# Kernel optimization log

Hardware: AMD Instinct MI355X
Metric: run time of the kernel (lower is better)

## Reference

```python
import jax, jax.numpy as jnp
from jax import lax
import numpy as np

INPUT_SIZE, HIDDEN_SIZE, OUTPUT_SIZE = 256, 2048, 128
NUM_STEPS = 8192
ALPHA = 0.1


def setup_inputs() -> dict:
    key = jax.random.key(0)
    ks = jax.random.split(key, 8)
    s_i = 1.0 / np.sqrt(INPUT_SIZE)
    s_h = 1.0 / np.sqrt(HIDDEN_SIZE)
    return {
        "input_sig": jax.random.normal(ks[0], (INPUT_SIZE, NUM_STEPS), jnp.float32),
        "rate": jax.random.uniform(ks[1], (HIDDEN_SIZE,), jnp.float32, -1.0, 1.0),
        "Wi": jax.random.uniform(ks[2], (HIDDEN_SIZE, INPUT_SIZE), jnp.float32, -s_i, s_i),
        "bi": jax.random.uniform(ks[3], (HIDDEN_SIZE,), jnp.float32, -s_i, s_i),
        "Wh": jax.random.uniform(ks[4], (HIDDEN_SIZE, HIDDEN_SIZE), jnp.float32, -s_h, s_h),
        "bh": jax.random.uniform(ks[5], (HIDDEN_SIZE,), jnp.float32, -s_h, s_h),
        "Wo": jax.random.uniform(ks[6], (OUTPUT_SIZE, HIDDEN_SIZE), jnp.float32, -s_h, s_h),
        "bo": jax.random.uniform(ks[7], (OUTPUT_SIZE,), jnp.float32, -s_h, s_h),
    }


def reference(input_sig, rate, Wi, bi, Wh, bh, Wo, bo):
    # Precompute input projection for all steps at once: (T, H)
    xproj = input_sig.T @ Wi.T + bi  # einsum 'ti,hi->th'

    def step(r, xp):
        r_new = jnp.tanh(xp + r @ Wh.T + bh)
        r = (1.0 - ALPHA) * r + ALPHA * r_new
        return r, r

    _, rates = lax.scan(step, rate, xproj)  # rates: (T, H)
    rate_all = rates.T                      # (H, T), matches torch stack(dim=1)
    logits = rates @ Wo.T + bo              # (T, O)
    output = jax.nn.log_softmax(logits.T, axis=0)  # LogSoftmax over classes
    return output, rate_all
```

## Files before the change

kernel.cpp:

```cpp
#include <hip/hip_runtime.h>
#include <math.h>

#define T_STEPS 8192
#define HID     2048
#define IN_SZ   256
#define OUT_SZ  128
#define NBLK    64
#define NTHR    512
#define RPB     32
#define SCRUB   0xFFFFFFFF00000000ull

typedef unsigned long long u64;
typedef unsigned int u32;
typedef __attribute__((ext_vector_type(4))) u32 u32x4;


__global__ void k_init(const float* __restrict__ rate, u64* ring) {
    int i = blockIdx.x * blockDim.x + threadIdx.x;
    if (i < HID) {
        ring[i] = (u64)__float_as_uint(rate[i]);
        ring[HID + i]     = SCRUB;
        ring[2 * HID + i] = SCRUB;
    }
}

__global__ void __launch_bounds__(256) k_xproj(const float* __restrict__ sig,
                                               const float* __restrict__ Wi,
                                               const float* __restrict__ bi,
                                               float* __restrict__ out2) {
    __shared__ float wl[32 * IN_SZ];
    const int tid = threadIdx.x;
    const int t0 = blockIdx.x * 512;
    const int h0 = blockIdx.y * 32;

    {
        const float4* s4 = (const float4*)(Wi + (size_t)h0 * IN_SZ);
        float4* d4 = (float4*)wl;
        #pragma unroll
        for (int k = 0; k < 8; ++k) d4[tid + k * 256] = s4[tid + k * 256];
    }
    __syncthreads();

    const int t1 = t0 + tid, t2 = t1 + 256;
    float acc1[32], acc2[32];
    #pragma unroll
    for (int j = 0; j < 32; ++j) { acc1[j] = 0.f; acc2[j] = 0.f; }

    for (int i = 0; i < IN_SZ; ++i) {
        float s1 = sig[(size_t)i * T_STEPS + t1];
        float s2 = sig[(size_t)i * T_STEPS + t2];
        #pragma unroll
        for (int j = 0; j < 32; ++j) {
            float w = wl[j * IN_SZ + i];
            acc1[j] = fmaf(w, s1, acc1[j]);
            acc2[j] = fmaf(w, s2, acc2[j]);
        }
    }
    #pragma unroll
    for (int j = 0; j < 32; ++j) {
        float b = bi[h0 + j];
        out2[(size_t)(h0 + j) * T_STEPS + t1] = acc1[j] + b;
        out2[(size_t)(h0 + j) * T_STEPS + t2] = acc2[j] + b;
    }
}

#define DECLROW(p) \
    float p##_0,  p##_1,  p##_2,  p##_3,  p##_4,  p##_5,  p##_6,  p##_7,  \
          p##_8,  p##_9,  p##_10, p##_11, p##_12, p##_13, p##_14, p##_15, \
          p##_16, p##_17, p##_18, p##_19, p##_20, p##_21, p##_22, p##_23, \
          p##_24, p##_25, p##_26, p##_27, p##_28, p##_29, p##_30, p##_31

#define SCAT(v, a, b, c, d) a = (v).x; b = (v).y; c = (v).z; d = (v).w

#define PIN8(a,b,c,d,e,f,g,h) \
    asm volatile("" : "+v"(a), "+v"(b), "+v"(c), "+v"(d), \
                      "+v"(e), "+v"(f), "+v"(g), "+v"(h))

#define PINROW(p) \
    PIN8(p##_0,  p##_1,  p##_2,  p##_3,  p##_4,  p##_5,  p##_6,  p##_7);  \
    PIN8(p##_8,  p##_9,  p##_10, p##_11, p##_12, p##_13, p##_14, p##_15); \
    PIN8(p##_16, p##_17, p##_18, p##_19, p##_20, p##_21, p##_22, p##_23); \
    PIN8(p##_24, p##_25, p##_26, p##_27, p##_28, p##_29, p##_30, p##_31)

#define DOTC(c, s0, s1, s2, s3) { \
    float4 rv = r4[(c) * 64 + lane]; \
    float4 av = a4[(c) * 64 + lane]; \
    float4 bv = b4[(c) * 64 + lane]; \
    p0 = fmaf(rv.x, av.x, p0); p0 = fmaf(rv.y, av.y, p0); \
    p0 = fmaf(rv.z, av.z, p0); p0 = fmaf(rv.w, av.w, p0); \
    p1 = fmaf(rv.x, bv.x, p1); p1 = fmaf(rv.y, bv.y, p1); \
    p1 = fmaf(rv.z, bv.z, p1); p1 = fmaf(rv.w, bv.w, p1); \
    p2 = fmaf(rv.x, wc_##s0, p2); p2 = fmaf(rv.y, wc_##s1, p2); \
    p2 = fmaf(rv.z, wc_##s2, p2); p2 = fmaf(rv.w, wc_##s3, p2); \
    p3 = fmaf(rv.x, wd_##s0, p3); p3 = fmaf(rv.y, wd_##s1, p3); \
    p3 = fmaf(rv.z, wd_##s2, p3); p3 = fmaf(rv.w, wd_##s3, p3); }

__global__ void __launch_bounds__(512, 2) k_scan(const float* __restrict__ Wh,
                                                 const float* __restrict__ bh,
                                                 float* __restrict__ out2,
                                                 u64* ring) {
    __shared__ float whs[16 * HID];
    __shared__ float rl[HID];
    const int tid  = threadIdx.x;
    const int bid  = blockIdx.x;
    const int w    = tid >> 6;
    const int lane = tid & 63;
    const int h0   = bid * RPB;
    const int ra   = h0 + 4 * w;

    const float4* Wh4 = (const float4*)Wh;
    {
        float4* whs4 = (float4*)whs;
        #pragma unroll
        for (int rr = 0; rr < 16; ++rr) {
            int grow = h0 + 4 * (rr >> 1) + (rr & 1);
            whs4[rr * 512 + tid] = Wh4[(size_t)grow * 512 + tid];
        }
    }
    DECLROW(wc);
    DECLROW(wd);
    {
        const float4* rp = Wh4 + (size_t)(ra + 2) * 512;
        const float4* rq = Wh4 + (size_t)(ra + 3) * 512;
        float4 v;
        v = rp[0 * 64 + lane]; SCAT(v, wc_0,  wc_1,  wc_2,  wc_3);
        v = rp[1 * 64 + lane]; SCAT(v, wc_4,  wc_5,  wc_6,  wc_7);
        v = rp[2 * 64 + lane]; SCAT(v, wc_8,  wc_9,  wc_10, wc_11);
        v = rp[3 * 64 + lane]; SCAT(v, wc_12, wc_13, wc_14, wc_15);
        v = rp[4 * 64 + lane]; SCAT(v, wc_16, wc_17, wc_18, wc_19);
        v = rp[5 * 64 + lane]; SCAT(v, wc_20, wc_21, wc_22, wc_23);
        v = rp[6 * 64 + lane]; SCAT(v, wc_24, wc_25, wc_26, wc_27);
        v = rp[7 * 64 + lane]; SCAT(v, wc_28, wc_29, wc_30, wc_31);
        v = rq[0 * 64 + lane]; SCAT(v, wd_0,  wd_1,  wd_2,  wd_3);
        v = rq[1 * 64 + lane]; SCAT(v, wd_4,  wd_5,  wd_6,  wd_7);
        v = rq[2 * 64 + lane]; SCAT(v, wd_8,  wd_9,  wd_10, wd_11);
        v = rq[3 * 64 + lane]; SCAT(v, wd_12, wd_13, wd_14, wd_15);
        v = rq[4 * 64 + lane]; SCAT(v, wd_16, wd_17, wd_18, wd_19);
        v = rq[5 * 64 + lane]; SCAT(v, wd_20, wd_21, wd_22, wd_23);
        v = rq[6 * 64 + lane]; SCAT(v, wd_24, wd_25, wd_26, wd_27);
        v = rq[7 * 64 + lane]; SCAT(v, wd_28, wd_29, wd_30, wd_31);
    }
    PINROW(wc);
    PINROW(wd);

    const int myrow = ra + lane;
    float mybh = 0.f;
    if (lane < 4) mybh = bh[myrow];
    __syncthreads();

    int cur = 0;
    for (int t = 0; t < T_STEPS; ++t) {
        float xp = 0.f;
        size_t myidx = 0;
        if (lane < 4) {
            myidx = (size_t)myrow * T_STEPS + t;
            xp = out2[myidx];
        }

        {
            const u64* src = ring + (size_t)cur * HID;
            const u64* p0p = src + 4 * tid;
            const u64* p1p = p0p + 2;
            const u32 tt = (u32)t;
            u32x4 a0, a1;
            float f0, f1, f2, f3;
            int got = 0;
            for (int rounds = 0; rounds < 32; ++rounds) {
                asm volatile("global_load_dwordx4 %0, %2, off sc1\n\t"
                             "global_load_dwordx4 %1, %3, off sc1\n\t"
                             "s_waitcnt vmcnt(0)"
                             : "=&v"(a0), "=&v"(a1)
                             : "v"(p0p), "v"(p1p)
                             : "memory");
                __builtin_amdgcn_sched_barrier(0);
                if (a0.y == tt && a0.w == tt && a1.y == tt && a1.w == tt) {
                    f0 = __uint_as_float(a0.x);
                    f1 = __uint_as_float(a0.z);
                    f2 = __uint_as_float(a1.x);
                    f3 = __uint_as_float(a1.z);
                    got = 1;
                    break;
                }
            }
            if (!got) {
                u64 vals[4];
                unsigned pend = 0xFu;
                while (pend) {
                    #pragma unroll
                    for (int q = 0; q < 4; ++q) {
                        if (pend & (1u << q))
                            vals[q] = __hip_atomic_load(&p0p[q], __ATOMIC_RELAXED,
                                                        __HIP_MEMORY_SCOPE_AGENT);
                    }
                    #pragma unroll
                    for (int q = 0; q < 4; ++q) {
                        if ((pend & (1u << q)) && (u32)(vals[q] >> 32) == tt)
                            pend &= ~(1u << q);
                    }
                }
                f0 = __uint_as_float((u32)vals[0]);
                f1 = __uint_as_float((u32)vals[1]);
                f2 = __uint_as_float((u32)vals[2]);
                f3 = __uint_as_float((u32)vals[3]);
            }
            float4 v; v.x = f0; v.y = f1; v.z = f2; v.w = f3;
            ((float4*)rl)[tid] = v;
        }
        __syncthreads();

        float p0 = 0.f, p1 = 0.f, p2 = 0.f, p3 = 0.f;
        {
            const float4* r4 = (const float4*)rl;
            const float4* a4 = (const float4*)(whs + (size_t)(2 * w) * HID);
            const float4* b4 = a4 + 512;
            DOTC(0, 0,  1,  2,  3);
            DOTC(1, 4,  5,  6,  7);
            DOTC(2, 8,  9,  10, 11);
            DOTC(3, 12, 13, 14, 15);
            DOTC(4, 16, 17, 18, 19);
            DOTC(5, 20, 21, 22, 23);
            DOTC(6, 24, 25, 26, 27);
            DOTC(7, 28, 29, 30, 31);
        }
        #pragma unroll
        for (int off = 32; off >= 1; off >>= 1) {
            p0 += __shfl_xor(p0, off, 64);
            p1 += __shfl_xor(p1, off, 64);
            p2 += __shfl_xor(p2, off, 64);
            p3 += __shfl_xor(p3, off, 64);
        }

        const int nxt = (cur == 2) ? 0 : cur + 1;
        if (lane < 4) {
            float myp = (lane & 2) ? ((lane & 1) ? p3 : p2)
                                   : ((lane & 1) ? p1 : p0);
            float rold = rl[myrow];
            float v = myp + xp + mybh;
            float rn = 0.9f * rold + 0.1f * tanhf(v);
            out2[myidx] = rn;
            u64* dst = ring + (size_t)nxt * HID;
            const u64 tagbits = (u64)(u32)(t + 1) << 32;
            __hip_atomic_store(&dst[myrow], tagbits | __float_as_uint(rn),
                               __ATOMIC_RELAXED, __HIP_MEMORY_SCOPE_AGENT);
        }
        cur = nxt;
    }
}

__global__ void __launch_bounds__(512) k_logits(const float* __restrict__ out2,
                                                const float* __restrict__ Wo,
                                                const float* __restrict__ bo,
                                                float* __restrict__ out0) {
    __shared__ float wos[128 * 128];
    __shared__ float red[8 * 128];
    __shared__ float fin[128];
    const int tid  = threadIdx.x;
    const int w    = tid >> 6;
    const int lane = tid & 63;
    const int t0   = blockIdx.x * 128;
    const int ob   = w * 16;

    float acc0[16], acc1[16];
    #pragma unroll
    for (int j = 0; j < 16; ++j) { acc0[j] = 0.f; acc1[j] = 0.f; }

    for (int hb = 0; hb < HID / 128; ++hb) {
        __syncthreads();
        {
            const float4* wo4 = (const float4*)Wo;
            float4* ws4 = (float4*)wos;
            #pragma unroll
            for (int k = 0; k < 8; ++k) {
                int g = tid + k * 512;
                int o = g >> 5;
                int c = g & 31;
                ws4[g] = wo4[(size_t)o * (HID / 4) + hb * 32 + c];
            }
        }
        __syncthreads();
        for (int hh = 0; hh < 128; ++hh) {
            int h = hb * 128 + hh;
            float rA = out2[(size_t)h * T_STEPS + t0 + lane];
            float rB = out2[(size_t)h * T_STEPS + t0 + 64 + lane];
            #pragma unroll
            for (int j = 0; j < 16; ++j) {
                float wv = wos[(ob + j) * 128 + hh];
                acc0[j] = fmaf(wv, rA, acc0[j]);
                acc1[j] = fmaf(wv, rB, acc1[j]);
            }
        }
    }
    #pragma unroll
    for (int j = 0; j < 16; ++j) {
        float b = bo[ob + j];
        acc0[j] += b; acc1[j] += b;
    }

    float m0 = acc0[0], m1 = acc1[0];
    #pragma unroll
    for (int j = 1; j < 16; ++j) { m0 = fmaxf(m0, acc0[j]); m1 = fmaxf(m1, acc1[j]); }
    red[w * 128 + lane] = m0;
    red[w * 128 + 64 + lane] = m1;
    __syncthreads();
    if (tid < 128) {
        float m = red[tid];
        #pragma unroll
        for (int q = 1; q < 8; ++q) m = fmaxf(m, red[q * 128 + tid]);
        fin[tid] = m;
    }
    __syncthreads();
    float fm0 = fin[lane], fm1 = fin[64 + lane];
    float s0 = 0.f, s1 = 0.f;
    #pragma unroll
    for (int j = 0; j < 16; ++j) {
        s0 += expf(acc0[j] - fm0);
        s1 += expf(acc1[j] - fm1);
    }
    red[w * 128 + lane] = s0;
    red[w * 128 + 64 + lane] = s1;
    __syncthreads();
    if (tid < 128) {
        float s = 0.f;
        #pragma unroll
        for (int q = 0; q < 8; ++q) s += red[q * 128 + tid];
        fin[tid] = fin[tid] + logf(s);
    }
    __syncthreads();
    float L0 = fin[lane], L1 = fin[64 + lane];
    #pragma unroll
    for (int j = 0; j < 16; ++j) {
        out0[(size_t)(ob + j) * T_STEPS + t0 + lane]      = acc0[j] - L0;
        out0[(size_t)(ob + j) * T_STEPS + t0 + 64 + lane] = acc1[j] - L1;
    }
}

extern "C" void kernel_launch(void* const* d_in, const int* in_sizes, int n_in,
                              void* d_out, int out_size, void* d_ws, size_t ws_size,
                              hipStream_t stream) {
    const float* sig  = (const float*)d_in[0];
    const float* rate = (const float*)d_in[1];
    const float* Wi   = (const float*)d_in[2];
    const float* bi   = (const float*)d_in[3];
    const float* Wh   = (const float*)d_in[4];
    const float* bh   = (const float*)d_in[5];
    const float* Wo   = (const float*)d_in[6];
    const float* bo   = (const float*)d_in[7];

    float* out0 = (float*)d_out;
    float* out2 = out0 + (size_t)OUT_SZ * T_STEPS;

    u64* ring = (u64*)d_ws;

    hipLaunchKernelGGL(k_init, dim3(8), dim3(256), 0, stream, rate, ring);
    hipLaunchKernelGGL(k_xproj, dim3(T_STEPS / 512, HID / 32), dim3(256), 0, stream,
                       sig, Wi, bi, out2);

    void* args[] = {(void*)&Wh, (void*)&bh, (void*)&out2, (void*)&ring};
    hipLaunchCooperativeKernel((const void*)k_scan, dim3(NBLK), dim3(NTHR),
                               args, 0, stream);

    hipLaunchKernelGGL(k_logits, dim3(T_STEPS / 128), dim3(512), 0, stream,
                       out2, Wo, bo, out0);
}
```

Measured before the change: 17.72 ms.

## Spread recurrent scan over 128 blocks with all weights held in registers

Doubles the number of persistent scan blocks from 64 to 128, so each block owns 16 hidden rows instead of 32 and each wave owns 2 rows. Both rows per wave now live fully in registers, and the shared-memory copy of Wh and its LDS reads in the dot product are removed. This halves the per-step FMA and reduction work per block, but doubles the number of blocks that poll the global ring each step, which may raise contention on the cross-block synchronisation. It also requires all 128 blocks to be co-resident on the device.

Result: faster. 15.19 ms (-14.3%).

```diff
diff --git a/kernel.cpp b/kernel.cpp
--- a/kernel.cpp
+++ b/kernel.cpp
@@ -5,9 +5,9 @@
 #define HID     2048
 #define IN_SZ   256
 #define OUT_SZ  128
-#define NBLK    64
+#define NBLK    128
 #define NTHR    512
-#define RPB     32
+#define RPB     16
 #define SCRUB   0xFFFFFFFF00000000ull
 
 typedef unsigned long long u64;
@@ -82,77 +82,54 @@
     PIN8(p##_16, p##_17, p##_18, p##_19, p##_20, p##_21, p##_22, p##_23); \
     PIN8(p##_24, p##_25, p##_26, p##_27, p##_28, p##_29, p##_30, p##_31)
 
+#define LOADROW(p, base) { \
+    float4 v; \
+    v = (base)[0 * 64 + lane]; SCAT(v, p##_0,  p##_1,  p##_2,  p##_3);  \
+    v = (base)[1 * 64 + lane]; SCAT(v, p##_4,  p##_5,  p##_6,  p##_7);  \
+    v = (base)[2 * 64 + lane]; SCAT(v, p##_8,  p##_9,  p##_10, p##_11); \
+    v = (base)[3 * 64 + lane]; SCAT(v, p##_12, p##_13, p##_14, p##_15); \
+    v = (base)[4 * 64 + lane]; SCAT(v, p##_16, p##_17, p##_18, p##_19); \
+    v = (base)[5 * 64 + lane]; SCAT(v, p##_20, p##_21, p##_22, p##_23); \
+    v = (base)[6 * 64 + lane]; SCAT(v, p##_24, p##_25, p##_26, p##_27); \
+    v = (base)[7 * 64 + lane]; SCAT(v, p##_28, p##_29, p##_30, p##_31); }
+
 #define DOTC(c, s0, s1, s2, s3) { \
     float4 rv = r4[(c) * 64 + lane]; \
-    float4 av = a4[(c) * 64 + lane]; \
-    float4 bv = b4[(c) * 64 + lane]; \
-    p0 = fmaf(rv.x, av.x, p0); p0 = fmaf(rv.y, av.y, p0); \
-    p0 = fmaf(rv.z, av.z, p0); p0 = fmaf(rv.w, av.w, p0); \
-    p1 = fmaf(rv.x, bv.x, p1); p1 = fmaf(rv.y, bv.y, p1); \
-    p1 = fmaf(rv.z, bv.z, p1); p1 = fmaf(rv.w, bv.w, p1); \
-    p2 = fmaf(rv.x, wc_##s0, p2); p2 = fmaf(rv.y, wc_##s1, p2); \
-    p2 = fmaf(rv.z, wc_##s2, p2); p2 = fmaf(rv.w, wc_##s3, p2); \
-    p3 = fmaf(rv.x, wd_##s0, p3); p3 = fmaf(rv.y, wd_##s1, p3); \
-    p3 = fmaf(rv.z, wd_##s2, p3); p3 = fmaf(rv.w, wd_##s3, p3); }
+    p0 = fmaf(rv.x, wa_##s0, p0); p0 = fmaf(rv.y, wa_##s1, p0); \
+    p0 = fmaf(rv.z, wa_##s2, p0); p0 = fmaf(rv.w, wa_##s3, p0); \
+    p1 = fmaf(rv.x, wb_##s0, p1); p1 = fmaf(rv.y, wb_##s1, p1); \
+    p1 = fmaf(rv.z, wb_##s2, p1); p1 = fmaf(rv.w, wb_##s3, p1); }
 
 __global__ void __launch_bounds__(512, 2) k_scan(const float* __restrict__ Wh,
                                                  const float* __restrict__ bh,
                                                  float* __restrict__ out2,
                                                  u64* ring) {
-    __shared__ float whs[16 * HID];
     __shared__ float rl[HID];
     const int tid  = threadIdx.x;
     const int bid  = blockIdx.x;
     const int w    = tid >> 6;
     const int lane = tid & 63;
     const int h0   = bid * RPB;
-    const int ra   = h0 + 4 * w;
+    const int ra   = h0 + 2 * w;
 
     const float4* Wh4 = (const float4*)Wh;
-    {
-        float4* whs4 = (float4*)whs;
-        #pragma unroll
-        for (int rr = 0; rr < 16; ++rr) {
-            int grow = h0 + 4 * (rr >> 1) + (rr & 1);
-            whs4[rr * 512 + tid] = Wh4[(size_t)grow * 512 + tid];
-        }
-    }
-    DECLROW(wc);
-    DECLROW(wd);
-    {
-        const float4* rp = Wh4 + (size_t)(ra + 2) * 512;
-        const float4* rq = Wh4 + (size_t)(ra + 3) * 512;
-        float4 v;
-        v = rp[0 * 64 + lane]; SCAT(v, wc_0,  wc_1,  wc_2,  wc_3);
-        v = rp[1 * 64 + lane]; SCAT(v, wc_4,  wc_5,  wc_6,  wc_7);
-        v = rp[2 * 64 + lane]; SCAT(v, wc_8,  wc_9,  wc_10, wc_11);
-        v = rp[3 * 64 + lane]; SCAT(v, wc_12, wc_13, wc_14, wc_15);
-        v = rp[4 * 64 + lane]; SCAT(v, wc_16, wc_17, wc_18, wc_19);
-        v = rp[5 * 64 + lane]; SCAT(v, wc_20, wc_21, wc_22, wc_23);
-        v = rp[6 * 64 + lane]; SCAT(v, wc_24, wc_25, wc_26, wc_27);
-        v = rp[7 * 64 + lane]; SCAT(v, wc_28, wc_29, wc_30, wc_31);
-        v = rq[0 * 64 + lane]; SCAT(v, wd_0,  wd_1,  wd_2,  wd_3);
-        v = rq[1 * 64 + lane]; SCAT(v, wd_4,  wd_5,  wd_6,  wd_7);
-        v = rq[2 * 64 + lane]; SCAT(v, wd_8,  wd_9,  wd_10, wd_11);
-        v = rq[3 * 64 + lane]; SCAT(v, wd_12, wd_13, wd_14, wd_15);
-        v = rq[4 * 64 + lane]; SCAT(v, wd_16, wd_17, wd_18, wd_19);
-        v = rq[5 * 64 + lane]; SCAT(v, wd_20, wd_21, wd_22, wd_23);
-        v = rq[6 * 64 + lane]; SCAT(v, wd_24, wd_25, wd_26, wd_27);
-        v = rq[7 * 64 + lane]; SCAT(v, wd_28, wd_29, wd_30, wd_31);
-    }
-    PINROW(wc);
-    PINROW(wd);
+    DECLROW(wa);
+    DECLROW(wb);
+    LOADROW(wa, Wh4 + (size_t)ra * 512);
+    LOADROW(wb, Wh4 + (size_t)(ra + 1) * 512);
+    PINROW(wa);
+    PINROW(wb);
 
     const int myrow = ra + lane;
     float mybh = 0.f;
-    if (lane < 4) mybh = bh[myrow];
+    if (lane < 2) mybh = bh[myrow];
     __syncthreads();
 
     int cur = 0;
     for (int t = 0; t < T_STEPS; ++t) {
         float xp = 0.f;
         size_t myidx = 0;
-        if (lane < 4) {
+        if (lane < 2) {
             myidx = (size_t)myrow * T_STEPS + t;
             xp = out2[myidx];
         }
@@ -208,11 +185,9 @@
         }
         __syncthreads();
 
-        float p0 = 0.f, p1 = 0.f, p2 = 0.f, p3 = 0.f;
+        float p0 = 0.f, p1 = 0.f;
         {
             const float4* r4 = (const float4*)rl;
-            const float4* a4 = (const float4*)(whs + (size_t)(2 * w) * HID);
-            const float4* b4 = a4 + 512;
             DOTC(0, 0,  1,  2,  3);
             DOTC(1, 4,  5,  6,  7);
             DOTC(2, 8,  9,  10, 11);
@@ -226,14 +201,11 @@
         for (int off = 32; off >= 1; off >>= 1) {
             p0 += __shfl_xor(p0, off, 64);
             p1 += __shfl_xor(p1, off, 64);
-            p2 += __shfl_xor(p2, off, 64);
-            p3 += __shfl_xor(p3, off, 64);
         }
 
         const int nxt = (cur == 2) ? 0 : cur + 1;
-        if (lane < 4) {
-            float myp = (lane & 2) ? ((lane & 1) ? p3 : p2)
-                                   : ((lane & 1) ? p1 : p0);
+        if (lane < 2) {
+            float myp = (lane & 1) ? p1 : p0;
             float rold = rl[myrow];
             float v = myp + xp + mybh;
             float rn = 0.9f * rold + 0.1f * tanhf(v);
```
